# Kernel optimization log

Hardware: AMD Instinct MI355X
Metric: run time of the kernel (lower is better)

The kernel has to match this reference:

```python
import jax, jax.numpy as jnp
import numpy as np


def setup_inputs() -> dict:
    key = jax.random.key(0)
    k1, k2, k3 = jax.random.split(key, 3)
    B, S, H, E = 4, 4096, 7168, 256
    return {
        "hidden_states": jax.random.normal(k1, (B, S, H), dtype=jnp.float32),
        "gate_weight": jax.random.normal(k2, (E, H), dtype=jnp.float32) * (H ** -0.5),
        "bias": jax.random.normal(k3, (E,), dtype=jnp.float32) * 0.01,
        "n_group": 8,
        "topk_group": 4,
        "top_k": 8,
    }


def reference(hidden_states, gate_weight, bias, n_group, topk_group, top_k):
    B, S, H = hidden_states.shape
    E = gate_weight.shape[0]
    group_size = E // n_group
    x = hidden_states.reshape(-1, H)  # [T, H]
    logits = jnp.einsum("th,eh->te", x, gate_weight)  # [T, E]
    scores = jax.nn.sigmoid(logits) + bias  # [T, E]
    scores_g = scores.reshape(-1, n_group, group_size)  # [T, G, E/G]
    group_scores = scores_g.max(axis=-1)  # [T, G]
    _, sel_groups = jax.lax.top_k(group_scores, topk_group)  # [T, topk_group]
    # group mask: 1.0 for selected groups (indices are distinct, so sum of one-hots is 0/1)
    group_mask = jax.nn.one_hot(sel_groups, n_group, dtype=scores.dtype).sum(axis=1)  # [T, G]
    masked = (scores_g * group_mask[:, :, None]).reshape(-1, E)  # [T, E]
    weights, indices = jax.lax.top_k(masked, top_k)  # [T, top_k]
    weights = weights / (weights.sum(axis=-1, keepdims=True) + 1e-6)
    return weights.reshape(B, S, -1), indices.reshape(B, S, -1)
```

## Files before the change

### kernel.cpp

```cpp
#include <hip/hip_runtime.h>


#define TTOK 16384
#define EEXP 256
#define HDIM 7168
#define BM 32
#define BK 128
#define NSTEP (HDIM / BK)
#define NTHR 256
#define NKC (HDIM / 32)
#define LDS_BYTES 33024

typedef __attribute__((ext_vector_type(4))) float f32x4;
typedef __attribute__((ext_vector_type(4))) _Float16 h4;
typedef __attribute__((ext_vector_type(8))) _Float16 h8;

__global__ __launch_bounds__(64) void pack_w_kernel(const float* __restrict__ W,
                                                    _Float16* __restrict__ whi,
                                                    _Float16* __restrict__ wlo) {
  const int kc = blockIdx.x;
  const int eb = blockIdx.y;
  const int lane = threadIdx.x;
  const int e = eb * 16 + (lane & 15);
  const int k0 = kc * 32 + (lane >> 4) * 8;
  const float* src = W + (size_t)e * HDIM + k0;
  h8 hi, lo;
#pragma unroll
  for (int j = 0; j < 8; ++j) {
    float x = src[j];
    _Float16 h = (_Float16)x;
    hi[j] = h;
    lo[j] = (_Float16)((x - (float)h) * 2048.0f);
  }
  const size_t fi = ((size_t)(eb * NKC + kc) * 64 + lane) * 8;
  *(h8*)(whi + fi) = hi;
  *(h8*)(wlo + fi) = lo;
}

__global__ __launch_bounds__(NTHR) void gate_kernel(
    const float* __restrict__ X, const _Float16* __restrict__ Whi,
    const _Float16* __restrict__ Wlo, const float* __restrict__ bias,
    float* __restrict__ outw, float* __restrict__ outi) {
  extern __shared__ char smem[];
  _Float16* Ahi = (_Float16*)smem;
  _Float16* Alo = (_Float16*)(smem + 8192);
  float (*scores)[EEXP + 1] = (float (*)[EEXP + 1])smem;

  const int tid = threadIdx.x;
  const int lane = tid & 63;
  const int wid = tid >> 6;
  const int webase = wid * 4;
  const int tok0 = blockIdx.x * BM;

  f32x4 ra[4];
  h8 bh0[4], bl0[4];
  h8 bh1[4], bl1[4];

  f32x4 acc1[2][4], acc2[2][4];
#pragma unroll
  for (int m = 0; m < 2; ++m)
#pragma unroll
    for (int n = 0; n < 4; ++n) {
      acc1[m][n] = (f32x4){0.f, 0.f, 0.f, 0.f};
      acc2[m][n] = (f32x4){0.f, 0.f, 0.f, 0.f};
    }

  auto LOADA = [&](int k0) {
#pragma unroll
    for (int i = 0; i < 4; ++i) {
      const int p = tid + i * 256;
      ra[i] = *(const f32x4*)(X + (size_t)(tok0 + (p >> 5)) * HDIM + k0 + (p & 31) * 4);
    }
  };

  auto STOREA = [&]() {
#pragma unroll
    for (int i = 0; i < 4; ++i) {
      const int p = tid + i * 256;
      const int row = p >> 5, q = p & 31;
      h4 hi, lo;
#pragma unroll
      for (int j = 0; j < 4; ++j) {
        float x = ra[i][j];
        _Float16 h = (_Float16)x;
        hi[j] = h;
        lo[j] = (_Float16)((x - (float)h) * 2048.0f);
      }
      const int ix = row * BK + (((q >> 1) ^ (row & 15)) << 3) + (q & 1) * 4;
      *(h4*)(Ahi + ix) = hi;
      *(h4*)(Alo + ix) = lo;
    }
  };

#define BLOAD(BH, BL, KC)                                              \
  {                                                                    \
    const int kc_ = (KC);                                              \
    _Pragma("unroll") for (int n = 0; n < 4; ++n) {                    \
      const long fi_ = ((long)(webase + n) * NKC + kc_) * 64 + lane;   \
      BH[n] = *(const h8*)(Whi + fi_ * 8);                             \
      BL[n] = *(const h8*)(Wlo + fi_ * 8);                             \
    }                                                                  \
  }

#define PHASE(S, BH, BL)                                                        \
  {                                                                             \
    h8 ah[2], al[2];                                                            \
    _Pragma("unroll") for (int m = 0; m < 2; ++m) {                             \
      const int r_ = m * 16 + (lane & 15);                                      \
      const int cc_ = (S) * 4 + (lane >> 4);                                    \
      const int ix_ = r_ * BK + ((cc_ ^ (r_ & 15)) << 3);                       \
      ah[m] = *(h8*)(Ahi + ix_);                                                \
      al[m] = *(h8*)(Alo + ix_);                                                \
    }                                                                           \
    _Pragma("unroll") for (int n = 0; n < 4; ++n)                               \
        _Pragma("unroll") for (int m = 0; m < 2; ++m) {                         \
      acc1[m][n] = __builtin_amdgcn_mfma_f32_16x16x32_f16(ah[m], BH[n], acc1[m][n], 0, 0, 0); \
      acc2[m][n] = __builtin_amdgcn_mfma_f32_16x16x32_f16(ah[m], BL[n], acc2[m][n], 0, 0, 0); \
      acc2[m][n] = __builtin_amdgcn_mfma_f32_16x16x32_f16(al[m], BH[n], acc2[m][n], 0, 0, 0); \
    }                                                                           \
  }

  LOADA(0);
  BLOAD(bh0, bl0, 0);
#pragma unroll 1
  for (int kk = 0; kk < NSTEP; ++kk) {
    __syncthreads();
    STOREA();
    __syncthreads();
    if (kk + 1 < NSTEP) LOADA((kk + 1) * BK);
    const int kcb = kk * 4;
    BLOAD(bh1, bl1, kcb + 1);
    PHASE(0, bh0, bl0);
    BLOAD(bh0, bl0, kcb + 2);
    PHASE(1, bh1, bl1);
    BLOAD(bh1, bl1, kcb + 3);
    PHASE(2, bh0, bl0);
    if (kk + 1 < NSTEP) { BLOAD(bh0, bl0, kcb + 4); }
    PHASE(3, bh1, bl1);
  }

  __syncthreads();

  const int ebase = wid * 64;
#pragma unroll
  for (int m = 0; m < 2; ++m)
#pragma unroll
    for (int n = 0; n < 4; ++n) {
      const int e = ebase + n * 16 + (lane & 15);
      const float b = bias[e];
      const int t0 = m * 16 + (lane >> 4) * 4;
#pragma unroll
      for (int r = 0; r < 4; ++r) {
        const float logit = acc1[m][n][r] + acc2[m][n][r] * (1.0f / 2048.0f);
        scores[t0 + r][e] = 1.0f / (1.0f + expf(-logit)) + b;
      }
    }
  __syncthreads();

  if ((lane & 7) == 0) {
    const int t = wid * 8 + (lane >> 3);
    const float* sc = scores[t];

    float gmax[8];
#pragma unroll
    for (int g = 0; g < 8; ++g) {
      float mx = -1e30f;
      for (int j = 0; j < 32; ++j) mx = fmaxf(mx, sc[g * 32 + j]);
      gmax[g] = mx;
    }
    unsigned selmask = 0;
    for (int it = 0; it < 4; ++it) {
      float best = -1e30f;
      int bi = 0;
      for (int g = 0; g < 8; ++g)
        if (!((selmask >> g) & 1) && gmax[g] > best) {
          best = gmax[g];
          bi = g;
        }
      selmask |= 1u << bi;
    }
    float vals[8];
    int idx[8];
#pragma unroll
    for (int j = 0; j < 8; ++j) {
      vals[j] = -1e30f;
      idx[j] = 0;
    }
    for (int e = 0; e < 256; ++e) {
      float v = ((selmask >> (e >> 5)) & 1) ? sc[e] : 0.0f;
      if (v > vals[7]) {
        int p = 7;
        while (p > 0 && v > vals[p - 1]) {
          vals[p] = vals[p - 1];
          idx[p] = idx[p - 1];
          --p;
        }
        vals[p] = v;
        idx[p] = e;
      }
    }
    float ssum = 0.0f;
#pragma unroll
    for (int j = 0; j < 8; ++j) ssum += vals[j];
    const float den = ssum + 1e-6f;
    const long tg = (long)tok0 + t;
#pragma unroll
    for (int j = 0; j < 8; ++j) {
      outw[tg * 8 + j] = vals[j] / den;
      outi[tg * 8 + j] = (float)idx[j];
    }
  }
}

extern "C" void kernel_launch(void* const* d_in, const int* in_sizes, int n_in,
                              void* d_out, int out_size, void* d_ws, size_t ws_size,
                              hipStream_t stream) {
  const float* X = (const float*)d_in[0];
  const float* W = (const float*)d_in[1];
  const float* bias = (const float*)d_in[2];

  _Float16* whi = (_Float16*)d_ws;
  _Float16* wlo = whi + (size_t)EEXP * HDIM;

  float* outw = (float*)d_out;
  float* outi = outw + (size_t)TTOK * 8;

  hipFuncSetAttribute((const void*)gate_kernel,
                      hipFuncAttributeMaxDynamicSharedMemorySize, LDS_BYTES);

  pack_w_kernel<<<dim3(NKC, EEXP / 16), 64, 0, stream>>>(W, whi, wlo);
  gate_kernel<<<TTOK / BM, NTHR, LDS_BYTES, stream>>>(X, whi, wlo, bias, outw, outi);
}
```

Measured before the change: 332.4 us.

## Split-K the gate GEMM and move sigmoid/top-k into a separate epilogue kernel

Splits the hidden dimension into two slices so the gate kernel launches twice as many blocks, each writing fp32 partial logits to a workspace buffer. A new epilogue kernel sums the two partials, applies sigmoid and bias, and runs the grouped top-k selection. Gate LDS drops to 16 KB and launch bounds request 4 blocks per SM for higher occupancy. The cost is an extra kernel launch and a round trip through global memory for 2x16384x256 floats.

```diff
diff --git a/kernel.cpp b/kernel.cpp
--- a/kernel.cpp
+++ b/kernel.cpp
@@ -6,10 +6,14 @@
 #define HDIM 7168
 #define BM 32
 #define BK 128
-#define NSTEP (HDIM / BK)
+#define SPLITK 2
+#define KSLICE (HDIM / SPLITK)
+#define NSTEP (KSLICE / BK)
 #define NTHR 256
 #define NKC (HDIM / 32)
-#define LDS_BYTES 33024
+#define KCPS (NKC / SPLITK)
+#define GATE_LDS 16384
+#define EPI_LDS (64 * 257 * 4)
 
 typedef __attribute__((ext_vector_type(4))) float f32x4;
 typedef __attribute__((ext_vector_type(4))) _Float16 h4;
@@ -37,20 +41,24 @@
   *(h8*)(wlo + fi) = lo;
 }
 
-__global__ __launch_bounds__(NTHR) void gate_kernel(
+__global__ __launch_bounds__(NTHR, 4) void gate_kernel(
     const float* __restrict__ X, const _Float16* __restrict__ Whi,
-    const _Float16* __restrict__ Wlo, const float* __restrict__ bias,
-    float* __restrict__ outw, float* __restrict__ outi) {
+    const _Float16* __restrict__ Wlo, float* __restrict__ part) {
   extern __shared__ char smem[];
   _Float16* Ahi = (_Float16*)smem;
   _Float16* Alo = (_Float16*)(smem + 8192);
-  float (*scores)[EEXP + 1] = (float (*)[EEXP + 1])smem;
+
+  const int bid = blockIdx.x;
+  const int slice = (bid & 7) >> 2;
+  const int tb = ((bid >> 3) << 2) | (bid & 3);
+  const int tok0 = tb * BM;
+  const int kbase = slice * KSLICE;
+  const int kcbase = slice * KCPS;
 
   const int tid = threadIdx.x;
   const int lane = tid & 63;
   const int wid = tid >> 6;
   const int webase = wid * 4;
-  const int tok0 = blockIdx.x * BM;
 
   f32x4 ra[4];
   h8 bh0[4], bl0[4];
@@ -120,15 +128,15 @@
     }                                                                           \
   }
 
-  LOADA(0);
-  BLOAD(bh0, bl0, 0);
+  LOADA(kbase);
+  BLOAD(bh0, bl0, kcbase);
 #pragma unroll 1
   for (int kk = 0; kk < NSTEP; ++kk) {
     __syncthreads();
     STOREA();
     __syncthreads();
-    if (kk + 1 < NSTEP) LOADA((kk + 1) * BK);
-    const int kcb = kk * 4;
+    if (kk + 1 < NSTEP) LOADA(kbase + (kk + 1) * BK);
+    const int kcb = kcbase + kk * 4;
     BLOAD(bh1, bl1, kcb + 1);
     PHASE(0, bh0, bl0);
     BLOAD(bh0, bl0, kcb + 2);
@@ -139,33 +147,50 @@
     PHASE(3, bh1, bl1);
   }
 
-  __syncthreads();
-
+  float* pbase = part + ((long)slice * TTOK + tok0) * EEXP;
   const int ebase = wid * 64;
 #pragma unroll
   for (int m = 0; m < 2; ++m)
 #pragma unroll
     for (int n = 0; n < 4; ++n) {
       const int e = ebase + n * 16 + (lane & 15);
-      const float b = bias[e];
       const int t0 = m * 16 + (lane >> 4) * 4;
 #pragma unroll
-      for (int r = 0; r < 4; ++r) {
-        const float logit = acc1[m][n][r] + acc2[m][n][r] * (1.0f / 2048.0f);
-        scores[t0 + r][e] = 1.0f / (1.0f + expf(-logit)) + b;
-      }
-    }
+      for (int r = 0; r < 4; ++r)
+        pbase[(long)(t0 + r) * EEXP + e] = acc1[m][n][r] + acc2[m][n][r] * (1.0f / 2048.0f);
+    }
+}
+
+__global__ __launch_bounds__(256) void epilogue_kernel(
+    const float* __restrict__ part, const float* __restrict__ bias,
+    float* __restrict__ outw, float* __restrict__ outi) {
+  extern __shared__ float sc[];
+  const int tid = threadIdx.x;
+  const long t0 = (long)blockIdx.x * 64;
+
+  const int e4 = (tid & 63) * 4;
+  const int rsub = tid >> 6;
+  const f32x4 bv = *(const f32x4*)(bias + e4);
+#pragma unroll
+  for (int rr = 0; rr < 16; ++rr) {
+    const int row = rr * 4 + rsub;
+    const f32x4 a = *(const f32x4*)(part + (t0 + row) * EEXP + e4);
+    const f32x4 c = *(const f32x4*)(part + ((long)TTOK + t0 + row) * EEXP + e4);
+#pragma unroll
+    for (int j = 0; j < 4; ++j) {
+      const float v = a[j] + c[j];
+      sc[row * 257 + e4 + j] = 1.0f / (1.0f + expf(-v)) + bv[j];
+    }
+  }
   __syncthreads();
 
-  if ((lane & 7) == 0) {
-    const int t = wid * 8 + (lane >> 3);
-    const float* sc = scores[t];
-
+  if (tid < 64) {
+    const float* s = sc + tid * 257;
     float gmax[8];
 #pragma unroll
     for (int g = 0; g < 8; ++g) {
       float mx = -1e30f;
-      for (int j = 0; j < 32; ++j) mx = fmaxf(mx, sc[g * 32 + j]);
+      for (int j = 0; j < 32; ++j) mx = fmaxf(mx, s[g * 32 + j]);
       gmax[g] = mx;
     }
     unsigned selmask = 0;
@@ -187,7 +212,7 @@
       idx[j] = 0;
     }
     for (int e = 0; e < 256; ++e) {
-      float v = ((selmask >> (e >> 5)) & 1) ? sc[e] : 0.0f;
+      const float v = ((selmask >> (e >> 5)) & 1) ? s[e] : 0.0f;
       if (v > vals[7]) {
         int p = 7;
         while (p > 0 && v > vals[p - 1]) {
@@ -203,7 +228,7 @@
 #pragma unroll
     for (int j = 0; j < 8; ++j) ssum += vals[j];
     const float den = ssum + 1e-6f;
-    const long tg = (long)tok0 + t;
+    const long tg = t0 + tid;
 #pragma unroll
     for (int j = 0; j < 8; ++j) {
       outw[tg * 8 + j] = vals[j] / den;
@@ -221,13 +246,15 @@
 
   _Float16* whi = (_Float16*)d_ws;
   _Float16* wlo = whi + (size_t)EEXP * HDIM;
+  float* part = (float*)(wlo + (size_t)EEXP * HDIM);
 
   float* outw = (float*)d_out;
   float* outi = outw + (size_t)TTOK * 8;
 
-  hipFuncSetAttribute((const void*)gate_kernel,
-                      hipFuncAttributeMaxDynamicSharedMemorySize, LDS_BYTES);
+  hipFuncSetAttribute((const void*)epilogue_kernel,
+                      hipFuncAttributeMaxDynamicSharedMemorySize, EPI_LDS);
 
   pack_w_kernel<<<dim3(NKC, EEXP / 16), 64, 0, stream>>>(W, whi, wlo);
-  gate_kernel<<<TTOK / BM, NTHR, LDS_BYTES, stream>>>(X, whi, wlo, bias, outw, outi);
-}
+  gate_kernel<<<SPLITK * (TTOK / BM), NTHR, GATE_LDS, stream>>>(X, whi, wlo, part);
+  epilogue_kernel<<<TTOK / 64, 256, EPI_LDS, stream>>>(part, bias, outw, outi);
+}
```

After: 1.115 ms. +235.6%, slower.

## Deepen weight-fragment prefetch to four buffers and use raw barriers with MFMA priority

Applied to the files above, without the earlier changes.

The global weight-fragment prefetch becomes a four-deep register ring, loading two k-chunks ahead instead of one, to hide more global-load latency behind the MFMA phases. The __syncthreads calls are replaced by a bare s_barrier, or by lgkmcnt(0) followed by s_barrier, so barriers no longer wait on outstanding global loads. MFMA blocks are bracketed with s_setprio, and launch bounds request 2 blocks per CU. The extra prefetch registers may be hard to fit within the occupancy bound, risking spills or lower occupancy. The first barrier in each iteration has no waitcnt, so it relies on LDS reads from the previous phase having completed.

```diff
diff --git a/kernel.cpp b/kernel.cpp
--- a/kernel.cpp
+++ b/kernel.cpp
@@ -14,6 +14,13 @@
 typedef __attribute__((ext_vector_type(4))) float f32x4;
 typedef __attribute__((ext_vector_type(4))) _Float16 h4;
 typedef __attribute__((ext_vector_type(8))) _Float16 h8;
+
+#define BAR_ONLY() asm volatile("s_barrier" ::: "memory")
+#define LGKM0_BAR()                                     \
+  do {                                                  \
+    asm volatile("s_waitcnt lgkmcnt(0)" ::: "memory");  \
+    asm volatile("s_barrier" ::: "memory");             \
+  } while (0)
 
 __global__ __launch_bounds__(64) void pack_w_kernel(const float* __restrict__ W,
                                                     _Float16* __restrict__ whi,
@@ -37,7 +44,7 @@
   *(h8*)(wlo + fi) = lo;
 }
 
-__global__ __launch_bounds__(NTHR) void gate_kernel(
+__global__ __launch_bounds__(NTHR, 2) void gate_kernel(
     const float* __restrict__ X, const _Float16* __restrict__ Whi,
     const _Float16* __restrict__ Wlo, const float* __restrict__ bias,
     float* __restrict__ outw, float* __restrict__ outi) {
@@ -55,6 +62,8 @@
   f32x4 ra[4];
   h8 bh0[4], bl0[4];
   h8 bh1[4], bl1[4];
+  h8 bh2[4], bl2[4];
+  h8 bh3[4], bl3[4];
 
   f32x4 acc1[2][4], acc2[2][4];
 #pragma unroll
@@ -112,34 +121,37 @@
       ah[m] = *(h8*)(Ahi + ix_);                                                \
       al[m] = *(h8*)(Alo + ix_);                                                \
     }                                                                           \
+    __builtin_amdgcn_s_setprio(1);                                              \
     _Pragma("unroll") for (int n = 0; n < 4; ++n)                               \
         _Pragma("unroll") for (int m = 0; m < 2; ++m) {                         \
       acc1[m][n] = __builtin_amdgcn_mfma_f32_16x16x32_f16(ah[m], BH[n], acc1[m][n], 0, 0, 0); \
       acc2[m][n] = __builtin_amdgcn_mfma_f32_16x16x32_f16(ah[m], BL[n], acc2[m][n], 0, 0, 0); \
       acc2[m][n] = __builtin_amdgcn_mfma_f32_16x16x32_f16(al[m], BH[n], acc2[m][n], 0, 0, 0); \
     }                                                                           \
+    __builtin_amdgcn_s_setprio(0);                                              \
   }
 
   LOADA(0);
   BLOAD(bh0, bl0, 0);
+  BLOAD(bh1, bl1, 1);
 #pragma unroll 1
   for (int kk = 0; kk < NSTEP; ++kk) {
-    __syncthreads();
+    BAR_ONLY();
     STOREA();
-    __syncthreads();
+    LGKM0_BAR();
     if (kk + 1 < NSTEP) LOADA((kk + 1) * BK);
     const int kcb = kk * 4;
-    BLOAD(bh1, bl1, kcb + 1);
+    BLOAD(bh2, bl2, kcb + 2);
     PHASE(0, bh0, bl0);
-    BLOAD(bh0, bl0, kcb + 2);
+    BLOAD(bh3, bl3, kcb + 3);
     PHASE(1, bh1, bl1);
-    BLOAD(bh1, bl1, kcb + 3);
-    PHASE(2, bh0, bl0);
     if (kk + 1 < NSTEP) { BLOAD(bh0, bl0, kcb + 4); }
-    PHASE(3, bh1, bl1);
-  }
-
-  __syncthreads();
+    PHASE(2, bh2, bl2);
+    if (kk + 1 < NSTEP) { BLOAD(bh1, bl1, kcb + 5); }
+    PHASE(3, bh3, bl3);
+  }
+
+  LGKM0_BAR();
 
   const int ebase = wid * 64;
 #pragma unroll
@@ -187,7 +199,7 @@
       idx[j] = 0;
     }
     for (int e = 0; e < 256; ++e) {
-      float v = ((selmask >> (e >> 5)) & 1) ? sc[e] : 0.0f;
+      const float v = ((selmask >> (e >> 5)) & 1) ? sc[e] : 0.0f;
       if (v > vals[7]) {
         int p = 7;
         while (p > 0 && v > vals[p - 1]) {
```

After: 395.3 us. +18.9%, slower.

## Stage packed weights into LDS via async global_load_lds with double buffering

Applied to the files above, without the earlier changes.

Weights are repacked into a per-K-step contiguous blob and copied straight into LDS with global_load_lds, double-buffered alongside a double-buffered split-fp16 A tile. The tile grows to 64 tokens and 512 threads in a 2x4 wave grid, so weight traffic per token is halved and B fragments come from LDS rather than per-wave global loads. Loads for the next step overlap with compute, with one barrier per step. The cost is 160KB of LDS, which limits occupancy to one block per CU, and the fixed blob layout is hard-coded.

```diff
diff --git a/kernel.cpp b/kernel.cpp
--- a/kernel.cpp
+++ b/kernel.cpp
@@ -4,25 +4,29 @@
 #define TTOK 16384
 #define EEXP 256
 #define HDIM 7168
-#define BM 32
-#define BK 128
+#define BM 64
+#define BK 64
 #define NSTEP (HDIM / BK)
-#define NTHR 256
-#define NKC (HDIM / 32)
-#define LDS_BYTES 33024
+#define NTHR 512
+#define LDS_BYTES 163840
+#define ABASE 131072
 
 typedef __attribute__((ext_vector_type(4))) float f32x4;
-typedef __attribute__((ext_vector_type(4))) _Float16 h4;
 typedef __attribute__((ext_vector_type(8))) _Float16 h8;
 
+__device__ __forceinline__ void gload_lds16(const void* g, void* l) {
+  typedef const __attribute__((address_space(1))) unsigned int gu32;
+  typedef __attribute__((address_space(3))) unsigned int lu32;
+  __builtin_amdgcn_global_load_lds((gu32*)g, (lu32*)l, 16, 0, 0);
+}
+
 __global__ __launch_bounds__(64) void pack_w_kernel(const float* __restrict__ W,
-                                                    _Float16* __restrict__ whi,
-                                                    _Float16* __restrict__ wlo) {
-  const int kc = blockIdx.x;
+                                                    _Float16* __restrict__ blob) {
+  const int kcg = blockIdx.x;
   const int eb = blockIdx.y;
   const int lane = threadIdx.x;
   const int e = eb * 16 + (lane & 15);
-  const int k0 = kc * 32 + (lane >> 4) * 8;
+  const int k0 = kcg * 32 + (lane >> 4) * 8;
   const float* src = W + (size_t)e * HDIM + k0;
   h8 hi, lo;
 #pragma unroll
@@ -32,29 +36,30 @@
     hi[j] = h;
     lo[j] = (_Float16)((x - (float)h) * 2048.0f);
   }
-  const size_t fi = ((size_t)(eb * NKC + kc) * 64 + lane) * 8;
-  *(h8*)(whi + fi) = hi;
-  *(h8*)(wlo + fi) = lo;
-}
-
-__global__ __launch_bounds__(NTHR) void gate_kernel(
-    const float* __restrict__ X, const _Float16* __restrict__ Whi,
-    const _Float16* __restrict__ Wlo, const float* __restrict__ bias,
-    float* __restrict__ outw, float* __restrict__ outi) {
+  char* dst = (char*)blob + ((size_t)kcg * 32 + eb * 2) * 1024 + lane * 16;
+  *(h8*)dst = hi;
+  *(h8*)(dst + 1024) = lo;
+}
+
+__global__ __launch_bounds__(NTHR, 1) void gate_kernel(
+    const float* __restrict__ X, const _Float16* __restrict__ Wblob,
+    const float* __restrict__ bias, float* __restrict__ outw,
+    float* __restrict__ outi) {
   extern __shared__ char smem[];
-  _Float16* Ahi = (_Float16*)smem;
-  _Float16* Alo = (_Float16*)(smem + 8192);
   float (*scores)[EEXP + 1] = (float (*)[EEXP + 1])smem;
 
   const int tid = threadIdx.x;
   const int lane = tid & 63;
   const int wid = tid >> 6;
-  const int webase = wid * 4;
+  const int wr = wid >> 2;
+  const int wc = wid & 3;
   const int tok0 = blockIdx.x * BM;
 
-  f32x4 ra[4];
-  h8 bh0[4], bl0[4];
-  h8 bh1[4], bl1[4];
+  const int arow = tid >> 3, ac8 = tid & 7;
+  const float* asrc = X + (size_t)(tok0 + arow) * HDIM + ac8 * 8;
+  const int awoff = arow * 128 + ((ac8 ^ (arow & 7)) << 4);
+
+  f32x4 ra0, ra1;
 
   f32x4 acc1[2][4], acc2[2][4];
 #pragma unroll
@@ -65,90 +70,93 @@
       acc2[m][n] = (f32x4){0.f, 0.f, 0.f, 0.f};
     }
 
-  auto LOADA = [&](int k0) {
-#pragma unroll
-    for (int i = 0; i < 4; ++i) {
-      const int p = tid + i * 256;
-      ra[i] = *(const f32x4*)(X + (size_t)(tok0 + (p >> 5)) * HDIM + k0 + (p & 31) * 4);
-    }
+  auto LOADA = [&](int step) {
+    ra0 = *(const f32x4*)(asrc + (size_t)step * BK);
+    ra1 = *(const f32x4*)(asrc + (size_t)step * BK + 4);
   };
 
-  auto STOREA = [&]() {
-#pragma unroll
-    for (int i = 0; i < 4; ++i) {
-      const int p = tid + i * 256;
-      const int row = p >> 5, q = p & 31;
-      h4 hi, lo;
-#pragma unroll
-      for (int j = 0; j < 4; ++j) {
-        float x = ra[i][j];
-        _Float16 h = (_Float16)x;
-        hi[j] = h;
-        lo[j] = (_Float16)((x - (float)h) * 2048.0f);
-      }
-      const int ix = row * BK + (((q >> 1) ^ (row & 15)) << 3) + (q & 1) * 4;
-      *(h4*)(Ahi + ix) = hi;
-      *(h4*)(Alo + ix) = lo;
+  auto STAGEB = [&](int step, int buf) {
+    const char* gs = (const char*)Wblob + (size_t)step * 65536 + lane * 16;
+    char* lb = smem + buf * 65536;
+#pragma unroll
+    for (int i = 0; i < 8; ++i) {
+      const int gb = i * 8 + wid;
+      gload_lds16(gs + gb * 1024, lb + gb * 1024);
     }
   };
 
-#define BLOAD(BH, BL, KC)                                              \
-  {                                                                    \
-    const int kc_ = (KC);                                              \
-    _Pragma("unroll") for (int n = 0; n < 4; ++n) {                    \
-      const long fi_ = ((long)(webase + n) * NKC + kc_) * 64 + lane;   \
-      BH[n] = *(const h8*)(Whi + fi_ * 8);                             \
-      BL[n] = *(const h8*)(Wlo + fi_ * 8);                             \
-    }                                                                  \
-  }
-
-#define PHASE(S, BH, BL)                                                        \
+  auto ACONV = [&](int buf) {
+    h8 hi, lo;
+#pragma unroll
+    for (int j = 0; j < 4; ++j) {
+      float x = ra0[j];
+      _Float16 h = (_Float16)x;
+      hi[j] = h;
+      lo[j] = (_Float16)((x - (float)h) * 2048.0f);
+      float y = ra1[j];
+      _Float16 g = (_Float16)y;
+      hi[4 + j] = g;
+      lo[4 + j] = (_Float16)((y - (float)g) * 2048.0f);
+    }
+    char* ab = smem + ABASE + buf * 16384;
+    *(h8*)(ab + awoff) = hi;
+    *(h8*)(ab + 8192 + awoff) = lo;
+  };
+
+#define PHASE(S, BUF)                                                           \
   {                                                                             \
+    const char* ab = smem + ABASE + (BUF) * 16384;                              \
+    const char* bb = smem + (BUF) * 65536;                                      \
     h8 ah[2], al[2];                                                            \
     _Pragma("unroll") for (int m = 0; m < 2; ++m) {                             \
-      const int r_ = m * 16 + (lane & 15);                                      \
-      const int cc_ = (S) * 4 + (lane >> 4);                                    \
-      const int ix_ = r_ * BK + ((cc_ ^ (r_ & 15)) << 3);                       \
-      ah[m] = *(h8*)(Ahi + ix_);                                                \
-      al[m] = *(h8*)(Alo + ix_);                                                \
+      const int r_ = wr * 32 + m * 16 + (lane & 15);                            \
+      const int ao_ = r_ * 128 + ((((S) * 4 + (lane >> 4)) ^ (lane & 7)) << 4); \
+      ah[m] = *(const h8*)(ab + ao_);                                           \
+      al[m] = *(const h8*)(ab + 8192 + ao_);                                    \
+    }                                                                           \
+    h8 bh[4], bl[4];                                                            \
+    _Pragma("unroll") for (int n = 0; n < 4; ++n) {                             \
+      const int bo_ = (((S) * 16 + (wc * 4 + n)) * 2) * 1024 + lane * 16;       \
+      bh[n] = *(const h8*)(bb + bo_);                                           \
+      bl[n] = *(const h8*)(bb + bo_ + 1024);                                    \
     }                                                                           \
     _Pragma("unroll") for (int n = 0; n < 4; ++n)                               \
         _Pragma("unroll") for (int m = 0; m < 2; ++m) {                         \
-      acc1[m][n] = __builtin_amdgcn_mfma_f32_16x16x32_f16(ah[m], BH[n], acc1[m][n], 0, 0, 0); \
-      acc2[m][n] = __builtin_amdgcn_mfma_f32_16x16x32_f16(ah[m], BL[n], acc2[m][n], 0, 0, 0); \
-      acc2[m][n] = __builtin_amdgcn_mfma_f32_16x16x32_f16(al[m], BH[n], acc2[m][n], 0, 0, 0); \
+      acc1[m][n] = __builtin_amdgcn_mfma_f32_16x16x32_f16(ah[m], bh[n], acc1[m][n], 0, 0, 0); \
+      acc2[m][n] = __builtin_amdgcn_mfma_f32_16x16x32_f16(ah[m], bl[n], acc2[m][n], 0, 0, 0); \
+      acc2[m][n] = __builtin_amdgcn_mfma_f32_16x16x32_f16(al[m], bh[n], acc2[m][n], 0, 0, 0); \
     }                                                                           \
   }
 
   LOADA(0);
-  BLOAD(bh0, bl0, 0);
+  STAGEB(0, 0);
+  ACONV(0);
+  asm volatile("s_waitcnt vmcnt(0) lgkmcnt(0)" ::: "memory");
+  __builtin_amdgcn_s_barrier();
+
+  int buf = 0;
 #pragma unroll 1
   for (int kk = 0; kk < NSTEP; ++kk) {
-    __syncthreads();
-    STOREA();
-    __syncthreads();
-    if (kk + 1 < NSTEP) LOADA((kk + 1) * BK);
-    const int kcb = kk * 4;
-    BLOAD(bh1, bl1, kcb + 1);
-    PHASE(0, bh0, bl0);
-    BLOAD(bh0, bl0, kcb + 2);
-    PHASE(1, bh1, bl1);
-    BLOAD(bh1, bl1, kcb + 3);
-    PHASE(2, bh0, bl0);
-    if (kk + 1 < NSTEP) { BLOAD(bh0, bl0, kcb + 4); }
-    PHASE(3, bh1, bl1);
-  }
-
-  __syncthreads();
-
-  const int ebase = wid * 64;
+    const bool pf = (kk + 1 < NSTEP);
+    if (pf) {
+      LOADA(kk + 1);
+      STAGEB(kk + 1, buf ^ 1);
+    }
+    PHASE(0, buf);
+    PHASE(1, buf);
+    if (pf) ACONV(buf ^ 1);
+    asm volatile("s_waitcnt vmcnt(0) lgkmcnt(0)" ::: "memory");
+    __builtin_amdgcn_s_barrier();
+    buf ^= 1;
+  }
+
 #pragma unroll
   for (int m = 0; m < 2; ++m)
 #pragma unroll
     for (int n = 0; n < 4; ++n) {
-      const int e = ebase + n * 16 + (lane & 15);
+      const int e = (wc * 4 + n) * 16 + (lane & 15);
       const float b = bias[e];
-      const int t0 = m * 16 + (lane >> 4) * 4;
+      const int t0 = wr * 32 + m * 16 + (lane >> 4) * 4;
 #pragma unroll
       for (int r = 0; r < 4; ++r) {
         const float logit = acc1[m][n][r] + acc2[m][n][r] * (1.0f / 2048.0f);
@@ -187,7 +195,7 @@
       idx[j] = 0;
     }
     for (int e = 0; e < 256; ++e) {
-      float v = ((selmask >> (e >> 5)) & 1) ? sc[e] : 0.0f;
+      const float v = ((selmask >> (e >> 5)) & 1) ? sc[e] : 0.0f;
       if (v > vals[7]) {
         int p = 7;
         while (p > 0 && v > vals[p - 1]) {
@@ -219,8 +227,7 @@
   const float* W = (const float*)d_in[1];
   const float* bias = (const float*)d_in[2];
 
-  _Float16* whi = (_Float16*)d_ws;
-  _Float16* wlo = whi + (size_t)EEXP * HDIM;
+  _Float16* wblob = (_Float16*)d_ws;
 
   float* outw = (float*)d_out;
   float* outi = outw + (size_t)TTOK * 8;
@@ -228,6 +235,6 @@
   hipFuncSetAttribute((const void*)gate_kernel,
                       hipFuncAttributeMaxDynamicSharedMemorySize, LDS_BYTES);
 
-  pack_w_kernel<<<dim3(NKC, EEXP / 16), 64, 0, stream>>>(W, whi, wlo);
-  gate_kernel<<<TTOK / BM, NTHR, LDS_BYTES, stream>>>(X, whi, wlo, bias, outw, outi);
-}
+  pack_w_kernel<<<dim3(HDIM / 32, EEXP / 16), 64, 0, stream>>>(W, wblob);
+  gate_kernel<<<TTOK / BM, NTHR, LDS_BYTES, stream>>>(X, wblob, bias, outw, outi);
+}
```

After: 285.7 us. 1.16x faster.
